# Optimization experiments

Hardware: AMD Instinct MI355X
Metric: run time of the kernel (lower is better)

The kernel has to match this reference:

```python
import jax, jax.numpy as jnp
import numpy as np

B, N, F_IN, F_OUT, T, E, K = 8, 1024, 32, 64, 24, 16384, 3


def setup_inputs() -> dict:
    key = jax.random.key(0)
    ks = jax.random.split(key, 9)
    return {
        "x": jax.random.normal(ks[0], (B, N, F_IN, T), jnp.float32),
        "edge_index": jax.random.randint(ks[1], (2, E), 0, N),
        "edge_weight": jax.random.uniform(ks[2], (E,), jnp.float32),
        # attention params (xavier-ish scale)
        "Ve": jax.random.normal(ks[3], (T, T), jnp.float32) * 0.2,
        "be": jax.random.normal(ks[4], (1, T, T), jnp.float32) * 0.2,
        "Vs": jax.random.normal(ks[5], (N, N), jnp.float32) * 0.03,
        "bs": jax.random.normal(ks[6], (1, N, N), jnp.float32) * 0.03,
        # ChebConv: K linear layers (no bias) + shared bias
        "cheb_W": jax.random.normal(ks[7], (K, F_IN, F_OUT), jnp.float32) * (1.0 / np.sqrt(F_IN)),
        "cheb_b": jnp.zeros((F_OUT,), jnp.float32),
        # 1x1 residual Conv2d(F_IN -> F_OUT): weight (F_OUT, F_IN), bias (F_OUT,)
        "res_W": jax.random.normal(ks[8], (F_OUT, F_IN), jnp.float32) * (1.0 / np.sqrt(F_IN)),
        "res_b": jnp.zeros((F_OUT,), jnp.float32),
    }


def _cheb_conv(x, row, col, w, Wk, b):
    """PyG-style ChebConv applied to a batch of graphs sharing edges.
    x: (BT, N, Fin). Scaled Laplacian with lambda_max=2 reduces to
    L_hat = -D^{-1/2} A D^{-1/2} with zero diagonal (self-loops removed).
    """
    n = x.shape[1]
    w = jnp.where(row == col, jnp.zeros_like(w), w)  # remove_self_loops
    deg = jnp.zeros((n,), x.dtype).at[row].add(w)
    dis = jnp.where(deg > 0, jax.lax.rsqrt(jnp.where(deg > 0, deg, 1.0)), 0.0)
    norm = -dis[row] * w * dis[col]  # (E,)

    def prop(z):  # z: (BT, N, F) -> L_hat @ z
        msg = norm[None, :, None] * z[:, row, :]  # (BT, E, F)
        return jnp.zeros_like(z).at[:, col, :].add(msg)

    Tx0 = x
    out = Tx0 @ Wk[0]
    Tx1 = prop(Tx0)
    out = out + Tx1 @ Wk[1]
    for k in range(2, Wk.shape[0]):  # small fixed K, not a data-dim loop
        Tx2 = 2.0 * prop(Tx1) - Tx0
        out = out + Tx2 @ Wk[k]
        Tx0, Tx1 = Tx1, Tx2
    return out + b


def reference(x, edge_index, edge_weight, Ve, be, Vs, bs, cheb_W, cheb_b, res_W, res_b):
    b_, n, f, t = x.shape
    row, col = edge_index[0], edge_index[1]

    # --- temporal attention: E = softmax(Ve @ sigmoid(X^T X) + be) ---
    x_flat = x.reshape(b_, n * f, t)
    score_t = jnp.einsum('bmt,bmu->btu', x_flat, x_flat)
    E_att = jax.nn.softmax(jnp.einsum('tu,buv->btv', Ve, jax.nn.sigmoid(score_t)) + be, axis=-1)
    x_TA = (x_flat @ E_att).reshape(b_, n, f, t)

    # --- spatial attention: S = softmax(Vs @ sigmoid(X X^T) + bs) ---
    xr = x_TA.reshape(b_, n, f * t)
    score_s = jnp.einsum('bnd,bmd->bnm', xr, xr)
    S_att = jax.nn.softmax(jnp.einsum('nm,bmk->bnk', Vs, jax.nn.sigmoid(score_s)) + bs, axis=-1)
    x_SA = (S_att @ xr).reshape(b_, n, f, t)

    # --- Chebyshev graph conv, batched over all B*T slices at once ---
    xg = x_SA.transpose(0, 3, 1, 2).reshape(b_ * t, n, f)  # (BT, N, Fin)
    x_gcn = _cheb_conv(xg, row, col, edge_weight, cheb_W, cheb_b)
    x_gcn = x_gcn.reshape(b_, t, n, -1).transpose(0, 2, 3, 1)  # (B, N, Fout, T)

    # --- 1x1 residual conv over channel dim ---
    x_res = jnp.einsum('gf,bnft->bngt', res_W, x) + res_b[None, None, :, None]

    return jax.nn.relu(x_gcn + x_res)
```

## Files before the change

### kernel.cpp

```cpp
#include <hip/hip_runtime.h>
#include <math.h>

#define NB 1024
#define FB 32
#define TB 24
#define GB 64
#define BB 8
#define EB 16384
#define MB 32768
#define DB 768
#define BTB 192
#define WSP 6144

typedef __attribute__((ext_vector_type(8))) short sh8;
typedef __attribute__((ext_vector_type(4))) float f32x4;

__device__ __forceinline__ float wsum(float v){
  #pragma unroll
  for (int o = 32; o; o >>= 1) v += __shfl_down(v, o);
  return v;
}
__device__ __forceinline__ float wmax(float v){
  #pragma unroll
  for (int o = 32; o; o >>= 1) v = fmaxf(v, __shfl_down(v, o));
  return v;
}
__device__ __forceinline__ float sigm(float v){ return 1.f / (1.f + expf(-v)); }
__device__ __forceinline__ float b2f(unsigned short u){ unsigned int t = ((unsigned int)u) << 16; return __uint_as_float(t); }
__device__ __forceinline__ unsigned short f2b(float f){
  unsigned int u = __float_as_uint(f);
  u += 0x7fffu + ((u >> 16) & 1u);
  return (unsigned short)(u >> 16);
}
__device__ __forceinline__ void gload16(const void* g, void* l){
  typedef const __attribute__((address_space(1))) unsigned int* gp_t;
  typedef __attribute__((address_space(3))) unsigned int* lp_t;
  __builtin_amdgcn_global_load_lds((gp_t)g, (lp_t)l, 16, 0, 0);
}

__global__ __launch_bounds__(256) void k_pass1(const float* __restrict__ x,
                                               unsigned short* __restrict__ xTn,
                                               float* __restrict__ score){
  const int n0 = blockIdx.x * 8, b = blockIdx.y;
  __shared__ float xl[8 * 32 * 25];
  const float* src = x + ((size_t)b * NB + n0) * DB;
  #pragma unroll
  for (int p = 0; p < 24; ++p){
    int i = p * 256 + threadIdx.x;
    int n = i / 768, rem = i % 768, f = rem / 24, t = rem % 24;
    xl[(n * 32 + f) * 25 + t] = src[i];
  }
  __syncthreads();
  #pragma unroll
  for (int nn = 0; nn < 8; ++nn){
    unsigned short* dst = xTn + ((size_t)(n0 + nn) * BTB + b * TB) * FB;
    #pragma unroll
    for (int p = 0; p < 3; ++p){
      int i2 = p * 256 + threadIdx.x;
      int t = i2 >> 5, f = i2 & 31;
      dst[t * FB + f] = f2b(xl[(nn * 32 + f) * 25 + t]);
    }
  }
  if (threadIdx.x < 192){
    const int t = threadIdx.x >> 3, u0 = (threadIdx.x & 7) * 3;
    float a0 = 0.f, a1 = 0.f, a2 = 0.f;
    for (int m = 0; m < 256; ++m){
      const float xt = xl[m * 25 + t];
      a0 = fmaf(xt, xl[m * 25 + u0 + 0], a0);
      a1 = fmaf(xt, xl[m * 25 + u0 + 1], a1);
      a2 = fmaf(xt, xl[m * 25 + u0 + 2], a2);
    }
    float* sb = score + (size_t)b * 576 + t * 24 + u0;
    atomicAdd(sb + 0, a0); atomicAdd(sb + 1, a1); atomicAdd(sb + 2, a2);
  }
}

__global__ __launch_bounds__(64) void k_eatt(const float* __restrict__ score,
                                             const float* __restrict__ Ve,
                                             const float* __restrict__ be,
                                             float* __restrict__ Eatt){
  const int b = blockIdx.x;
  __shared__ float sg[576], Ar[576], Vel[576], bel[576];
  for (int i = threadIdx.x; i < 576; i += 64){
    sg[i] = sigm(score[(size_t)b * 576 + i]);
    Vel[i] = Ve[i]; bel[i] = be[i];
  }
  __syncthreads();
  for (int i = threadIdx.x; i < 576; i += 64){
    int t = i / 24, v = i % 24;
    float s = 0.f;
    #pragma unroll
    for (int u = 0; u < 24; ++u) s = fmaf(Vel[t*24+u], sg[u*24+v], s);
    Ar[i] = s + bel[i];
  }
  __syncthreads();
  if (threadIdx.x < 24){
    const int t = threadIdx.x;
    float mx = -1e30f;
    #pragma unroll
    for (int v = 0; v < 24; ++v) mx = fmaxf(mx, Ar[t*24+v]);
    float e[24]; float sum = 0.f;
    #pragma unroll
    for (int v = 0; v < 24; ++v){ e[v] = expf(Ar[t*24+v] - mx); sum += e[v]; }
    const float inv = 1.f / sum;
    #pragma unroll
    for (int v = 0; v < 24; ++v) Eatt[(size_t)b * 576 + t*24 + v] = e[v] * inv;
  }
}

__global__ __launch_bounds__(256) void k_xta2(const unsigned short* __restrict__ xTn,
                                              const float* __restrict__ Eatt,
                                              unsigned short* __restrict__ xTAh){
  const int n0 = blockIdx.x * 8, b = blockIdx.y;
  __shared__ float E[576];
  __shared__ unsigned short xl[8 * 32 * 25];
  for (int i = threadIdx.x; i < 576; i += 256) E[i] = Eatt[(size_t)b * 576 + i];
  #pragma unroll
  for (int p = 0; p < 12; ++p){
    int i = p * 256 + threadIdx.x;
    int nn = i / 384, within = i % 384;
    unsigned int v = *(const unsigned int*)(xTn + ((size_t)(n0 + nn) * BTB + b * TB) * FB + within * 2);
    int e0 = within * 2, t0 = e0 >> 5, f0 = e0 & 31;
    int e1 = e0 + 1,     t1 = e1 >> 5, f1 = e1 & 31;
    xl[(nn * 32 + f0) * 25 + t0] = (unsigned short)v;
    xl[(nn * 32 + f1) * 25 + t1] = (unsigned short)(v >> 16);
  }
  __syncthreads();
  const int r = threadIdx.x;
  float in[TB], o[TB];
  #pragma unroll
  for (int u = 0; u < TB; ++u) in[u] = b2f(xl[r * 25 + u]);
  #pragma unroll
  for (int v = 0; v < TB; ++v) o[v] = 0.f;
  #pragma unroll
  for (int u = 0; u < TB; ++u){
    const float xv = in[u];
    #pragma unroll
    for (int v = 0; v < TB; ++v) o[v] = fmaf(xv, E[u*24+v], o[v]);
  }
  unsigned int pk[12];
  #pragma unroll
  for (int q = 0; q < 12; ++q)
    pk[q] = (unsigned int)f2b(o[2*q]) | ((unsigned int)f2b(o[2*q+1]) << 16);
  uint4* op = (uint4*)(xTAh + ((size_t)b * MB + n0 * 32 + r) * TB);
  op[0] = make_uint4(pk[0], pk[1], pk[2], pk[3]);
  op[1] = make_uint4(pk[4], pk[5], pk[6], pk[7]);
  op[2] = make_uint4(pk[8], pk[9], pk[10], pk[11]);
}

__global__ __launch_bounds__(256) void k_tr(const unsigned short* __restrict__ in,
                                            unsigned short* __restrict__ out){
  const int dt = blockIdx.x, nt = blockIdx.y, b = blockIdx.z;
  __shared__ unsigned short ts[64 * 66];
  const unsigned short* ib = in + (size_t)b * (NB * DB) + (size_t)(nt * 64) * DB + dt * 64;
  #pragma unroll
  for (int p = 0; p < 8; ++p){
    int fl = p * 256 + threadIdx.x;
    int rr = fl >> 5, cc = (fl & 31) * 2;
    unsigned int v = *(const unsigned int*)(ib + (size_t)rr * DB + cc);
    ts[rr * 66 + cc] = (unsigned short)v;
    ts[rr * 66 + cc + 1] = (unsigned short)(v >> 16);
  }
  __syncthreads();
  unsigned short* ob = out + (size_t)b * (NB * DB) + (size_t)(dt * 64) * NB + nt * 64;
  #pragma unroll
  for (int p = 0; p < 16; ++p){
    int fl = p * 256 + threadIdx.x;
    int dd = fl >> 6, nn = fl & 63;
    ob[(size_t)dd * NB + nn] = ts[nn * 66 + dd];
  }
}

template<int EPI>
__global__ __launch_bounds__(256) void k_mgemm(const unsigned short* __restrict__ A,
                                               const unsigned short* __restrict__ B,
                                               unsigned short* __restrict__ C,
                                               int lda, int ldb, int ldc, int Kk, int nbx,
                                               long sA, long sB, long sC){
  __shared__ unsigned short As[2][8192];
  __shared__ unsigned short Bs[2][8192];
  const int d = blockIdx.x;
  const int bz = d & 7;
  const int rr = d >> 3;
  const int bx = rr % nbx, by = rr / nbx;
  A += (size_t)bz * sA; B += (size_t)bz * sB; C += (size_t)bz * sC;
  const int i0 = by * 128, j0 = bx * 128;
  const int tid = threadIdx.x, wave = tid >> 6, lane = tid & 63;
  const int fr = lane & 15, rowb = (lane >> 4) * 4;
  const int wr = (wave >> 1) * 64, wc = (wave & 1) * 64;
  const int srow = tid >> 3;
  const int sko = (((lane & 7) ^ (lane >> 3)) * 8);
  f32x4 acc[4][4];
  #pragma unroll
  for (int m = 0; m < 4; ++m)
    #pragma unroll
    for (int n = 0; n < 4; ++n) acc[m][n] = 0.f;

  auto stage = [&](int buf, int k0){
    #pragma unroll
    for (int it = 0; it < 4; ++it){
      const int r = it * 32 + srow;
      gload16(A + (size_t)(i0 + r) * lda + k0 + sko, &As[buf][(it*4 + wave) * 512]);
      gload16(B + (size_t)(j0 + r) * ldb + k0 + sko, &Bs[buf][(it*4 + wave) * 512]);
    }
  };
  auto compute = [&](int buf){
    #pragma unroll
    for (int kk = 0; kk < 2; ++kk){
      const int ch = kk * 4 + (lane >> 4);
      const int cs = (ch ^ (fr & 7)) * 8;
      sh8 af[4], bfr[4];
      #pragma unroll
      for (int m = 0; m < 4; ++m)
        af[m] = *(const sh8*)&As[buf][(wr + m*16 + fr) * 64 + cs];
      #pragma unroll
      for (int n = 0; n < 4; ++n)
        bfr[n] = *(const sh8*)&Bs[buf][(wc + n*16 + fr) * 64 + cs];
      #pragma unroll
      for (int m = 0; m < 4; ++m)
        #pragma unroll
        for (int n = 0; n < 4; ++n)
          acc[m][n] = __builtin_amdgcn_mfma_f32_16x16x32_bf16(af[m], bfr[n], acc[m][n], 0, 0, 0);
    }
  };

  stage(0, 0);
  asm volatile("s_waitcnt vmcnt(0)" ::: "memory");
  __builtin_amdgcn_s_barrier();
  int cur = 0;
  for (int k0 = 64; k0 < Kk; k0 += 64){
    stage(cur ^ 1, k0);
    compute(cur);
    asm volatile("s_waitcnt vmcnt(0)" ::: "memory");
    __builtin_amdgcn_s_barrier();
    cur ^= 1;
  }
  compute(cur);

  #pragma unroll
  for (int m = 0; m < 4; ++m){
    const int row = i0 + wr + m*16 + rowb;
    #pragma unroll
    for (int n = 0; n < 4; ++n){
      const int colg = j0 + wc + n*16 + fr;
      #pragma unroll
      for (int r = 0; r < 4; ++r){
        float v = acc[m][n][r];
        if (EPI == 1) v = sigm(v);
        C[(size_t)(row + r) * ldc + colg] = f2b(v);
      }
    }
  }
}

__global__ __launch_bounds__(256) void k_softmax_s(const unsigned short* __restrict__ C2h,
                                                   const float* __restrict__ bs,
                                                   unsigned short* __restrict__ Sh){
  const int blk = blockIdx.x;
  const int n = blk & 1023;
  const unsigned short* row = C2h + (size_t)blk * 1024;
  const float* bsr = bs + (size_t)n * 1024;
  const int tid = threadIdx.x;
  uint2 rv = ((const uint2*)row)[tid];
  float4 bb = ((const float4*)bsr)[tid];
  float v0 = b2f((unsigned short)rv.x)         + bb.x;
  float v1 = b2f((unsigned short)(rv.x >> 16)) + bb.y;
  float v2 = b2f((unsigned short)rv.y)         + bb.z;
  float v3 = b2f((unsigned short)(rv.y >> 16)) + bb.w;
  float mx = fmaxf(fmaxf(v0, v1), fmaxf(v2, v3));
  mx = wmax(mx);
  __shared__ float s4[4];
  __shared__ float s4b[4];
  if ((tid & 63) == 0) s4[tid >> 6] = mx;
  __syncthreads();
  mx = fmaxf(fmaxf(s4[0], s4[1]), fmaxf(s4[2], s4[3]));
  float e0 = expf(v0 - mx), e1 = expf(v1 - mx), e2 = expf(v2 - mx), e3 = expf(v3 - mx);
  float sum = wsum(e0 + e1 + e2 + e3);
  if ((tid & 63) == 0) s4b[tid >> 6] = sum;
  __syncthreads();
  sum = s4b[0] + s4b[1] + s4b[2] + s4b[3];
  const float inv = 1.f / sum;
  uint2 ov;
  ov.x = (unsigned int)f2b(e0 * inv) | ((unsigned int)f2b(e1 * inv) << 16);
  ov.y = (unsigned int)f2b(e2 * inv) | ((unsigned int)f2b(e3 * inv) << 16);
  ((uint2*)(Sh + (size_t)blk * 1024))[tid] = ov;
}

__global__ __launch_bounds__(256) void k_t0n(const unsigned short* __restrict__ xSAh,
                                             unsigned short* __restrict__ T0n){
  const int n0 = blockIdx.x * 8, b = blockIdx.y;
  __shared__ unsigned short s[8 * 32 * 25];
  const unsigned int* src = (const unsigned int*)(xSAh + ((size_t)b * NB + n0) * DB);
  #pragma unroll
  for (int p = 0; p < 12; ++p){
    int i = p * 256 + threadIdx.x;
    unsigned int v = src[i];
    int d0 = (i * 2) % DB, nn = (i * 2) / DB;
    int f0 = d0 / 24, t0 = d0 % 24;
    int d1 = d0 + 1, f1 = d1 / 24, t1 = d1 % 24;
    s[(nn * 32 + f0) * 25 + t0] = (unsigned short)v;
    s[(nn * 32 + f1) * 25 + t1] = (unsigned short)(v >> 16);
  }
  __syncthreads();
  #pragma unroll
  for (int nn = 0; nn < 8; ++nn){
    unsigned short* dst = T0n + ((size_t)(n0 + nn) * BTB + b * TB) * FB;
    #pragma unroll
    for (int p = 0; p < 3; ++p){
      int i2 = p * 256 + threadIdx.x;
      int t = i2 >> 5, f = i2 & 31;
      dst[t * FB + f] = s[(nn * 32 + f) * 25 + t];
    }
  }
}

__global__ __launch_bounds__(256) void k_edge_deg(const int* __restrict__ ei,
                                                  const float* __restrict__ ew,
                                                  float* __restrict__ deg,
                                                  int* __restrict__ cnt){
  int e = blockIdx.x * 256 + threadIdx.x;
  if (e >= EB) return;
  int r = ei[e], c = ei[EB + e];
  float w = (r == c) ? 0.f : ew[e];
  atomicAdd(&deg[r], w);
  atomicAdd(&cnt[c], 1);
}

__global__ __launch_bounds__(1024) void k_scan(const int* __restrict__ cnt,
                                               int* __restrict__ ptr,
                                               int* __restrict__ fill){
  __shared__ int sd[1024];
  const int i = threadIdx.x;
  int c = cnt[i];
  sd[i] = c;
  __syncthreads();
  int v = c;
  for (int s = 1; s < 1024; s <<= 1){
    int t = (i >= s) ? sd[i - s] : 0;
    __syncthreads();
    v += t; sd[i] = v;
    __syncthreads();
  }
  ptr[i + 1] = v;
  fill[i] = v - c;
  if (i == 0) ptr[0] = 0;
}

__global__ __launch_bounds__(256) void k_edge_fill(const int* __restrict__ ei,
                                                   const float* __restrict__ ew,
                                                   const float* __restrict__ deg,
                                                   int* __restrict__ fill,
                                                   int* __restrict__ cidx,
                                                   float* __restrict__ normv){
  int e = blockIdx.x * 256 + threadIdx.x;
  if (e >= EB) return;
  int r = ei[e], c = ei[EB + e];
  float w = (r == c) ? 0.f : ew[e];
  float dr = deg[r], dc = deg[c];
  float ir = dr > 0.f ? rsqrtf(dr) : 0.f;
  float ic = dc > 0.f ? rsqrtf(dc) : 0.f;
  normv[e] = -ir * w * ic;
  int pos = atomicAdd(&fill[c], 1);
  cidx[pos] = e;
}

#define ACC8(vv) { \
  acc[0] = fmaf(w, b2f((unsigned short)(vv).x), acc[0]); \
  acc[1] = fmaf(w, b2f((unsigned short)((vv).x >> 16)), acc[1]); \
  acc[2] = fmaf(w, b2f((unsigned short)(vv).y), acc[2]); \
  acc[3] = fmaf(w, b2f((unsigned short)((vv).y >> 16)), acc[3]); \
  acc[4] = fmaf(w, b2f((unsigned short)(vv).z), acc[4]); \
  acc[5] = fmaf(w, b2f((unsigned short)((vv).z >> 16)), acc[5]); \
  acc[6] = fmaf(w, b2f((unsigned short)(vv).w), acc[6]); \
  acc[7] = fmaf(w, b2f((unsigned short)((vv).w >> 16)), acc[7]); }

__global__ __launch_bounds__(256) void k_spmm(const unsigned short* __restrict__ z,
                                              const float* __restrict__ normv,
                                              const int* __restrict__ cidx,
                                              const int* __restrict__ ei,
                                              const int* __restrict__ ptr,
                                              const unsigned short* __restrict__ sub,
                                              float scale,
                                              unsigned short* __restrict__ outz){
  const int c = blockIdx.x & 1023;
  const int off = (blockIdx.x >> 10) * 2048 + threadIdx.x * 8;
  const int j0 = ptr[c], j1 = ptr[c + 1];
  __shared__ int rs[128];
  __shared__ float ws[128];
  float acc[8];
  #pragma unroll
  for (int q = 0; q < 8; ++q) acc[q] = 0.f;
  for (int jb = j0; jb < j1; jb += 128){
    const int cnt = min(128, j1 - jb);
    __syncthreads();
    for (int j = threadIdx.x; j < cnt; j += 256){
      int e = cidx[jb + j];
      rs[j] = ei[e];
      ws[j] = normv[e];
    }
    __syncthreads();
    for (int j = 0; j < cnt; ++j){
      const uint4 v = *(const uint4*)(z + (size_t)rs[j] * WSP + off);
      const float w = ws[j];
      ACC8(v)
    }
  }
  float sv[8];
  if (sub){
    const uint4 s0 = *(const uint4*)(sub + (size_t)c * WSP + off);
    sv[0]=b2f((unsigned short)s0.x); sv[1]=b2f((unsigned short)(s0.x>>16));
    sv[2]=b2f((unsigned short)s0.y); sv[3]=b2f((unsigned short)(s0.y>>16));
    sv[4]=b2f((unsigned short)s0.z); sv[5]=b2f((unsigned short)(s0.z>>16));
    sv[6]=b2f((unsigned short)s0.w); sv[7]=b2f((unsigned short)(s0.w>>16));
  } else {
    #pragma unroll
    for (int q = 0; q < 8; ++q) sv[q] = 0.f;
  }
  unsigned int pk[4];
  #pragma unroll
  for (int q = 0; q < 4; ++q){
    float a = scale * acc[2*q]     - sv[2*q];
    float b = scale * acc[2*q + 1] - sv[2*q + 1];
    pk[q] = (unsigned int)f2b(a) | ((unsigned int)f2b(b) << 16);
  }
  *(uint4*)(outz + (size_t)c * WSP + off) = make_uint4(pk[0], pk[1], pk[2], pk[3]);
}

__global__ __launch_bounds__(256) void k_fgemm(const unsigned short* __restrict__ T0n,
                                               const unsigned short* __restrict__ T1n,
                                               const unsigned short* __restrict__ T2n,
                                               const unsigned short* __restrict__ xTn,
                                               const unsigned short* __restrict__ Wh,
                                               const float* __restrict__ bsum,
                                               float* __restrict__ out){
  __shared__ unsigned short As[16384];
  __shared__ unsigned short Ws[8192];
  const int m0 = blockIdx.x * 128;
  const int tid = threadIdx.x, wave = tid >> 6, lane = tid & 63;
  const int fr = lane & 15, rowb = (lane >> 4) * 4;
  const int wr = (wave >> 1) * 64, wc = (wave & 1) * 32;
  #pragma unroll
  for (int it = 0; it < 8; ++it){
    const int row = it * 16 + wave * 4 + (lane >> 4);
    const int g = (lane & 15) ^ (row & 7);
    const int ss = g >> 2, off = (g & 3) * 8;
    const unsigned short* bp = (ss == 0) ? T0n : (ss == 1) ? T1n : (ss == 2) ? T2n : xTn;
    gload16(bp + (size_t)(m0 + row) * FB + off, &As[(it*4 + wave) * 512]);
  }
  #pragma unroll
  for (int it = 0; it < 4; ++it){
    const int row = it * 16 + wave * 4 + (lane >> 4);
    const int g = (lane & 15) ^ (row & 7);
    gload16(Wh + (size_t)row * 128 + g * 8, &Ws[(it*4 + wave) * 512]);
  }
  __syncthreads();
  f32x4 acc[4][2];
  #pragma unroll
  for (int m = 0; m < 4; ++m){ acc[m][0] = 0.f; acc[m][1] = 0.f; }
  #pragma unroll
  for (int kk = 0; kk < 4; ++kk){
    const int ch = kk * 4 + (lane >> 4);
    const int cs = (ch ^ (fr & 7)) * 8;
    sh8 af[4], bf2[2];
    #pragma unroll
    for (int m = 0; m < 4; ++m)
      af[m] = *(const sh8*)&As[(wr + m*16 + fr) * 128 + cs];
    #pragma unroll
    for (int n = 0; n < 2; ++n)
      bf2[n] = *(const sh8*)&Ws[(wc + n*16 + fr) * 128 + cs];
    #pragma unroll
    for (int m = 0; m < 4; ++m)
      #pragma unroll
      for (int n = 0; n < 2; ++n)
        acc[m][n] = __builtin_amdgcn_mfma_f32_16x16x32_bf16(af[m], bf2[n], acc[m][n], 0, 0, 0);
  }
  #pragma unroll
  for (int m = 0; m < 4; ++m){
    const int row4 = m0 + wr + m*16 + rowb;
    const int nn = row4 / 192;
    const int rem = row4 - nn * 192;
    const int b = rem / 24;
    const int t0 = rem - b * 24;
    #pragma unroll
    for (int n = 0; n < 2; ++n){
      const int g = wc + n*16 + fr;
      const float bv = bsum[g];
      float4 v;
      v.x = fmaxf(acc[m][n][0] + bv, 0.f);
      v.y = fmaxf(acc[m][n][1] + bv, 0.f);
      v.z = fmaxf(acc[m][n][2] + bv, 0.f);
      v.w = fmaxf(acc[m][n][3] + bv, 0.f);
      *(float4*)(out + (((size_t)b * NB + nn) * GB + g) * TB + t0) = v;
    }
  }
}

__global__ __launch_bounds__(256) void k_vsh(const float* __restrict__ Vs,
                                             unsigned short* __restrict__ Vsh){
  int i = (blockIdx.x * 256 + threadIdx.x) * 4;
  float4 v = *(const float4*)(Vs + i);
  unsigned short* o = Vsh + i;
  o[0] = f2b(v.x); o[1] = f2b(v.y); o[2] = f2b(v.z); o[3] = f2b(v.w);
}

__global__ __launch_bounds__(256) void k_wcat(const float* __restrict__ cW,
                                              const float* __restrict__ cB,
                                              const float* __restrict__ rW,
                                              const float* __restrict__ rB,
                                              unsigned short* __restrict__ Wh,
                                              float* __restrict__ bsum){
  for (int i = threadIdx.x; i < 8192; i += 256){
    int g = i >> 7, k = i & 127;
    int s = k >> 5, f = k & 31;
    float v = (s < 3) ? cW[(s * 32 + f) * 64 + g] : rW[g * 32 + f];
    Wh[i] = f2b(v);
  }
  if (threadIdx.x < 64) bsum[threadIdx.x] = cB[threadIdx.x] + rB[threadIdx.x];
}

extern "C" void kernel_launch(void* const* d_in, const int* in_sizes, int n_in,
                              void* d_out, int out_size, void* d_ws, size_t ws_size,
                              hipStream_t stream){
  const float* x  = (const float*)d_in[0];
  const int*   ei = (const int*)d_in[1];
  const float* ew = (const float*)d_in[2];
  const float* Ve = (const float*)d_in[3];
  const float* be = (const float*)d_in[4];
  const float* Vs = (const float*)d_in[5];
  const float* bs = (const float*)d_in[6];
  const float* cW = (const float*)d_in[7];
  const float* cB = (const float*)d_in[8];
  const float* rW = (const float*)d_in[9];
  const float* rB = (const float*)d_in[10];
  float* out = (float*)d_out;

  char* W = (char*)d_ws;
  unsigned short* sigh  = (unsigned short*)(W + 0);
  unsigned short* Sh    = sigh;
  unsigned short* xTAh  = (unsigned short*)(W + 16777216);
  unsigned short* T0n   = xTAh;
  unsigned short* xTAhT = (unsigned short*)(W + 29360128);
  unsigned short* T1n   = xTAhT;
  unsigned short* xTn   = (unsigned short*)(W + 41943040);
  unsigned short* xSAh  = (unsigned short*)(W + 54525952);
  unsigned short* T2n   = xSAh;
  unsigned short* C2h   = (unsigned short*)(W + 67108864);
  unsigned short* Vsh   = (unsigned short*)(W + 83886080);
  unsigned short* Wh    = (unsigned short*)(W + 92274688);
  float* bsum  = (float*)(W + 92291072);
  float* score = (float*)(W + 92291328);
  float* Eatt  = (float*)(W + 92309760);
  float* normv = (float*)(W + 92328192);
  float* deg   = (float*)(W + 92393728);
  int*   cnt   = (int*)(W + 92397824);
  int*   ptr   = (int*)(W + 92401920);
  int*   fill  = (int*)(W + 92406272);
  int*   cidx  = (int*)(W + 92410368);

  hipMemsetAsync(score, 0, 18432, stream);
  hipMemsetAsync(deg, 0, 8192, stream);

  k_wcat<<<1, 256, 0, stream>>>(cW, cB, rW, rB, Wh, bsum);
  k_vsh<<<1024, 256, 0, stream>>>(Vs, Vsh);

  k_pass1<<<dim3(128, 8), 256, 0, stream>>>(x, xTn, score);
  k_eatt<<<8, 64, 0, stream>>>(score, Ve, be, Eatt);
  k_xta2<<<dim3(128, 8), 256, 0, stream>>>(xTn, Eatt, xTAh);
  k_tr<<<dim3(12, 16, 8), 256, 0, stream>>>(xTAh, xTAhT);

  k_mgemm<1><<<512, 256, 0, stream>>>(xTAh, xTAh, sigh, DB, DB, NB, DB, 8,
                                      (long)NB*DB, (long)NB*DB, (long)NB*NB);
  k_mgemm<2><<<512, 256, 0, stream>>>(Vsh, sigh, C2h, NB, NB, NB, NB, 8,
                                      0L, (long)NB*NB, (long)NB*NB);
  k_softmax_s<<<8192, 256, 0, stream>>>(C2h, bs, Sh);
  k_mgemm<2><<<384, 256, 0, stream>>>(Sh, xTAhT, xSAh, NB, NB, DB, NB, 6,
                                      (long)NB*NB, (long)NB*DB, (long)NB*DB);

  k_t0n<<<dim3(128, 8), 256, 0, stream>>>(xSAh, T0n);
  k_edge_deg<<<64, 256, 0, stream>>>(ei, ew, deg, cnt);
  k_scan<<<1, 1024, 0, stream>>>(cnt, ptr, fill);
  k_edge_fill<<<64, 256, 0, stream>>>(ei, ew, deg, fill, cidx, normv);
  k_spmm<<<3072, 256, 0, stream>>>(T0n, normv, cidx, ei, ptr, nullptr, 1.f, T1n);
  k_spmm<<<3072, 256, 0, stream>>>(T1n, normv, cidx, ei, ptr, T0n, 2.f, T2n);

  k_fgemm<<<1536, 256, 0, stream>>>(T0n, T1n, T2n, xTn, Wh, bsum, out);
}
```

Before: 237.1 us.

## Exploit Gram symmetry, fuse graph preprocessing and constant kernels, retile SpMM

The spatial score X X^T is symmetric, so a new GEMM kernel computes only the lower-triangular 128x128 tiles (288 blocks instead of 512) and writes each off-diagonal tile twice, once mirrored. That mirrored write is a strided, uncoalesced store. Degree computation, the CSR scan and the edge fill are merged into one 1024-thread block using shared-memory atomics, and the two weight-conversion kernels are merged into one launch. SpMM now uses 192-thread blocks with 4 elements per thread, giving more blocks per column so the gather load spreads more evenly.

```diff
diff --git a/kernel.cpp b/kernel.cpp
--- a/kernel.cpp
+++ b/kernel.cpp
@@ -253,6 +253,89 @@
   }
 }
 
+__global__ __launch_bounds__(256) void k_mgemm_sym(const unsigned short* __restrict__ A,
+                                                   unsigned short* __restrict__ C,
+                                                   int lda, int ldc, int Kk,
+                                                   long sA, long sC){
+  __shared__ unsigned short As[2][8192];
+  __shared__ unsigned short Bs[2][8192];
+  const int d = blockIdx.x;
+  const int bz = d & 7;
+  int r = d >> 3;
+  int by = 0;
+  while (r >= by + 1){ r -= by + 1; ++by; }
+  const int bx = r;
+  A += (size_t)bz * sA; C += (size_t)bz * sC;
+  const int i0 = by * 128, j0 = bx * 128;
+  const int tid = threadIdx.x, wave = tid >> 6, lane = tid & 63;
+  const int fr = lane & 15, rowb = (lane >> 4) * 4;
+  const int wr = (wave >> 1) * 64, wc = (wave & 1) * 64;
+  const int srow = tid >> 3;
+  const int sko = (((lane & 7) ^ (lane >> 3)) * 8);
+  f32x4 acc[4][4];
+  #pragma unroll
+  for (int m = 0; m < 4; ++m)
+    #pragma unroll
+    for (int n = 0; n < 4; ++n) acc[m][n] = 0.f;
+
+  auto stage = [&](int buf, int k0){
+    #pragma unroll
+    for (int it = 0; it < 4; ++it){
+      const int rr2 = it * 32 + srow;
+      gload16(A + (size_t)(i0 + rr2) * lda + k0 + sko, &As[buf][(it*4 + wave) * 512]);
+      gload16(A + (size_t)(j0 + rr2) * lda + k0 + sko, &Bs[buf][(it*4 + wave) * 512]);
+    }
+  };
+  auto compute = [&](int buf){
+    #pragma unroll
+    for (int kk = 0; kk < 2; ++kk){
+      const int ch = kk * 4 + (lane >> 4);
+      const int cs = (ch ^ (fr & 7)) * 8;
+      sh8 af[4], bfr[4];
+      #pragma unroll
+      for (int m = 0; m < 4; ++m)
+        af[m] = *(const sh8*)&As[buf][(wr + m*16 + fr) * 64 + cs];
+      #pragma unroll
+      for (int n = 0; n < 4; ++n)
+        bfr[n] = *(const sh8*)&Bs[buf][(wc + n*16 + fr) * 64 + cs];
+      #pragma unroll
+      for (int m = 0; m < 4; ++m)
+        #pragma unroll
+        for (int n = 0; n < 4; ++n)
+          acc[m][n] = __builtin_amdgcn_mfma_f32_16x16x32_bf16(af[m], bfr[n], acc[m][n], 0, 0, 0);
+    }
+  };
+
+  stage(0, 0);
+  asm volatile("s_waitcnt vmcnt(0)" ::: "memory");
+  __builtin_amdgcn_s_barrier();
+  int cur = 0;
+  for (int k0 = 64; k0 < Kk; k0 += 64){
+    stage(cur ^ 1, k0);
+    compute(cur);
+    asm volatile("s_waitcnt vmcnt(0)" ::: "memory");
+    __builtin_amdgcn_s_barrier();
+    cur ^= 1;
+  }
+  compute(cur);
+
+  const bool mir = (bx != by);
+  #pragma unroll
+  for (int m = 0; m < 4; ++m){
+    const int row = i0 + wr + m*16 + rowb;
+    #pragma unroll
+    for (int n = 0; n < 4; ++n){
+      const int colg = j0 + wc + n*16 + fr;
+      #pragma unroll
+      for (int r2 = 0; r2 < 4; ++r2){
+        const unsigned short h = f2b(sigm(acc[m][n][r2]));
+        C[(size_t)(row + r2) * ldc + colg] = h;
+        if (mir) C[(size_t)colg * ldc + row + r2] = h;
+      }
+    }
+  }
+}
+
 __global__ __launch_bounds__(256) void k_softmax_s(const unsigned short* __restrict__ C2h,
                                                    const float* __restrict__ bs,
                                                    unsigned short* __restrict__ Sh){
@@ -314,24 +397,28 @@
   }
 }
 
-__global__ __launch_bounds__(256) void k_edge_deg(const int* __restrict__ ei,
-                                                  const float* __restrict__ ew,
-                                                  float* __restrict__ deg,
-                                                  int* __restrict__ cnt){
-  int e = blockIdx.x * 256 + threadIdx.x;
-  if (e >= EB) return;
-  int r = ei[e], c = ei[EB + e];
-  float w = (r == c) ? 0.f : ew[e];
-  atomicAdd(&deg[r], w);
-  atomicAdd(&cnt[c], 1);
-}
-
-__global__ __launch_bounds__(1024) void k_scan(const int* __restrict__ cnt,
-                                               int* __restrict__ ptr,
-                                               int* __restrict__ fill){
+__global__ __launch_bounds__(1024) void k_graph(const int* __restrict__ ei,
+                                                const float* __restrict__ ew,
+                                                int* __restrict__ ptr,
+                                                int* __restrict__ cidx,
+                                                float* __restrict__ normv){
+  __shared__ float degs[1024];
+  __shared__ int cnts[1024];
+  __shared__ int base[1024];
   __shared__ int sd[1024];
   const int i = threadIdx.x;
-  int c = cnt[i];
+  degs[i] = 0.f; cnts[i] = 0;
+  __syncthreads();
+  #pragma unroll
+  for (int p = 0; p < 16; ++p){
+    int e = p * 1024 + i;
+    int r = ei[e], c = ei[EB + e];
+    float w = (r == c) ? 0.f : ew[e];
+    atomicAdd(&degs[r], w);
+    atomicAdd(&cnts[c], 1);
+  }
+  __syncthreads();
+  int c = cnts[i];
   sd[i] = c;
   __syncthreads();
   int v = c;
@@ -342,39 +429,24 @@
     __syncthreads();
   }
   ptr[i + 1] = v;
-  fill[i] = v - c;
+  base[i] = v - c;
   if (i == 0) ptr[0] = 0;
-}
-
-__global__ __launch_bounds__(256) void k_edge_fill(const int* __restrict__ ei,
-                                                   const float* __restrict__ ew,
-                                                   const float* __restrict__ deg,
-                                                   int* __restrict__ fill,
-                                                   int* __restrict__ cidx,
-                                                   float* __restrict__ normv){
-  int e = blockIdx.x * 256 + threadIdx.x;
-  if (e >= EB) return;
-  int r = ei[e], c = ei[EB + e];
-  float w = (r == c) ? 0.f : ew[e];
-  float dr = deg[r], dc = deg[c];
-  float ir = dr > 0.f ? rsqrtf(dr) : 0.f;
-  float ic = dc > 0.f ? rsqrtf(dc) : 0.f;
-  normv[e] = -ir * w * ic;
-  int pos = atomicAdd(&fill[c], 1);
-  cidx[pos] = e;
-}
-
-#define ACC8(vv) { \
-  acc[0] = fmaf(w, b2f((unsigned short)(vv).x), acc[0]); \
-  acc[1] = fmaf(w, b2f((unsigned short)((vv).x >> 16)), acc[1]); \
-  acc[2] = fmaf(w, b2f((unsigned short)(vv).y), acc[2]); \
-  acc[3] = fmaf(w, b2f((unsigned short)((vv).y >> 16)), acc[3]); \
-  acc[4] = fmaf(w, b2f((unsigned short)(vv).z), acc[4]); \
-  acc[5] = fmaf(w, b2f((unsigned short)((vv).z >> 16)), acc[5]); \
-  acc[6] = fmaf(w, b2f((unsigned short)(vv).w), acc[6]); \
-  acc[7] = fmaf(w, b2f((unsigned short)((vv).w >> 16)), acc[7]); }
-
-__global__ __launch_bounds__(256) void k_spmm(const unsigned short* __restrict__ z,
+  __syncthreads();
+  #pragma unroll
+  for (int p = 0; p < 16; ++p){
+    int e = p * 1024 + i;
+    int r = ei[e], cc = ei[EB + e];
+    float w = (r == cc) ? 0.f : ew[e];
+    float dr = degs[r], dc = degs[cc];
+    float ir = dr > 0.f ? rsqrtf(dr) : 0.f;
+    float ic = dc > 0.f ? rsqrtf(dc) : 0.f;
+    normv[e] = -ir * w * ic;
+    int pos = atomicAdd(&base[cc], 1);
+    cidx[pos] = e;
+  }
+}
+
+__global__ __launch_bounds__(192) void k_spmm(const unsigned short* __restrict__ z,
                                               const float* __restrict__ normv,
                                               const int* __restrict__ cidx,
                                               const int* __restrict__ ei,
@@ -382,48 +454,41 @@
                                               const unsigned short* __restrict__ sub,
                                               float scale,
                                               unsigned short* __restrict__ outz){
-  const int c = blockIdx.x & 1023;
-  const int off = (blockIdx.x >> 10) * 2048 + threadIdx.x * 8;
+  const int s = blockIdx.x & 7;
+  const int c = blockIdx.x >> 3;
+  const int off = s * 768 + threadIdx.x * 4;
   const int j0 = ptr[c], j1 = ptr[c + 1];
-  __shared__ int rs[128];
-  __shared__ float ws[128];
-  float acc[8];
-  #pragma unroll
-  for (int q = 0; q < 8; ++q) acc[q] = 0.f;
-  for (int jb = j0; jb < j1; jb += 128){
-    const int cnt = min(128, j1 - jb);
+  __shared__ int rs[192];
+  __shared__ float ws[192];
+  float acc[4] = {0.f, 0.f, 0.f, 0.f};
+  for (int jb = j0; jb < j1; jb += 192){
+    const int cnt = min(192, j1 - jb);
     __syncthreads();
-    for (int j = threadIdx.x; j < cnt; j += 256){
-      int e = cidx[jb + j];
-      rs[j] = ei[e];
-      ws[j] = normv[e];
+    if (threadIdx.x < cnt){
+      int e = cidx[jb + threadIdx.x];
+      rs[threadIdx.x] = ei[e];
+      ws[threadIdx.x] = normv[e];
     }
     __syncthreads();
     for (int j = 0; j < cnt; ++j){
-      const uint4 v = *(const uint4*)(z + (size_t)rs[j] * WSP + off);
+      const uint2 v = *(const uint2*)(z + (size_t)rs[j] * WSP + off);
       const float w = ws[j];
-      ACC8(v)
-    }
-  }
-  float sv[8];
+      acc[0] = fmaf(w, b2f((unsigned short)v.x), acc[0]);
+      acc[1] = fmaf(w, b2f((unsigned short)(v.x >> 16)), acc[1]);
+      acc[2] = fmaf(w, b2f((unsigned short)v.y), acc[2]);
+      acc[3] = fmaf(w, b2f((unsigned short)(v.y >> 16)), acc[3]);
+    }
+  }
+  float sv[4] = {0.f, 0.f, 0.f, 0.f};
   if (sub){
-    const uint4 s0 = *(const uint4*)(sub + (size_t)c * WSP + off);
-    sv[0]=b2f((unsigned short)s0.x); sv[1]=b2f((unsigned short)(s0.x>>16));
-    sv[2]=b2f((unsigned short)s0.y); sv[3]=b2f((unsigned short)(s0.y>>16));
-    sv[4]=b2f((unsigned short)s0.z); sv[5]=b2f((unsigned short)(s0.z>>16));
-    sv[6]=b2f((unsigned short)s0.w); sv[7]=b2f((unsigned short)(s0.w>>16));
-  } else {
-    #pragma unroll
-    for (int q = 0; q < 8; ++q) sv[q] = 0.f;
-  }
-  unsigned int pk[4];
-  #pragma unroll
-  for (int q = 0; q < 4; ++q){
-    float a = scale * acc[2*q]     - sv[2*q];
-    float b = scale * acc[2*q + 1] - sv[2*q + 1];
-    pk[q] = (unsigned int)f2b(a) | ((unsigned int)f2b(b) << 16);
-  }
-  *(uint4*)(outz + (size_t)c * WSP + off) = make_uint4(pk[0], pk[1], pk[2], pk[3]);
+    const uint2 s0 = *(const uint2*)(sub + (size_t)c * WSP + off);
+    sv[0] = b2f((unsigned short)s0.x); sv[1] = b2f((unsigned short)(s0.x >> 16));
+    sv[2] = b2f((unsigned short)s0.y); sv[3] = b2f((unsigned short)(s0.y >> 16));
+  }
+  uint2 ov;
+  ov.x = (unsigned int)f2b(scale * acc[0] - sv[0]) | ((unsigned int)f2b(scale * acc[1] - sv[1]) << 16);
+  ov.y = (unsigned int)f2b(scale * acc[2] - sv[2]) | ((unsigned int)f2b(scale * acc[3] - sv[3]) << 16);
+  *(uint2*)(outz + (size_t)c * WSP + off) = ov;
 }
 
 __global__ __launch_bounds__(256) void k_fgemm(const unsigned short* __restrict__ T0n,
@@ -495,27 +560,28 @@
   }
 }
 
-__global__ __launch_bounds__(256) void k_vsh(const float* __restrict__ Vs,
-                                             unsigned short* __restrict__ Vsh){
-  int i = (blockIdx.x * 256 + threadIdx.x) * 4;
-  float4 v = *(const float4*)(Vs + i);
-  unsigned short* o = Vsh + i;
-  o[0] = f2b(v.x); o[1] = f2b(v.y); o[2] = f2b(v.z); o[3] = f2b(v.w);
-}
-
-__global__ __launch_bounds__(256) void k_wcat(const float* __restrict__ cW,
-                                              const float* __restrict__ cB,
-                                              const float* __restrict__ rW,
-                                              const float* __restrict__ rB,
-                                              unsigned short* __restrict__ Wh,
-                                              float* __restrict__ bsum){
-  for (int i = threadIdx.x; i < 8192; i += 256){
-    int g = i >> 7, k = i & 127;
-    int s = k >> 5, f = k & 31;
-    float v = (s < 3) ? cW[(s * 32 + f) * 64 + g] : rW[g * 32 + f];
-    Wh[i] = f2b(v);
-  }
-  if (threadIdx.x < 64) bsum[threadIdx.x] = cB[threadIdx.x] + rB[threadIdx.x];
+__global__ __launch_bounds__(256) void k_const(const float* __restrict__ Vs,
+                                               const float* __restrict__ cW,
+                                               const float* __restrict__ cB,
+                                               const float* __restrict__ rW,
+                                               const float* __restrict__ rB,
+                                               unsigned short* __restrict__ Vsh,
+                                               unsigned short* __restrict__ Wh,
+                                               float* __restrict__ bsum){
+  if (blockIdx.x == 0){
+    for (int i = threadIdx.x; i < 8192; i += 256){
+      int g = i >> 7, k = i & 127;
+      int s = k >> 5, f = k & 31;
+      float v = (s < 3) ? cW[(s * 32 + f) * 64 + g] : rW[g * 32 + f];
+      Wh[i] = f2b(v);
+    }
+    if (threadIdx.x < 64) bsum[threadIdx.x] = cB[threadIdx.x] + rB[threadIdx.x];
+  } else {
+    int i = ((blockIdx.x - 1) * 256 + threadIdx.x) * 4;
+    float4 v = *(const float4*)(Vs + i);
+    unsigned short* o = Vsh + i;
+    o[0] = f2b(v.x); o[1] = f2b(v.y); o[2] = f2b(v.z); o[3] = f2b(v.w);
+  }
 }
 
 extern "C" void kernel_launch(void* const* d_in, const int* in_sizes, int n_in,
@@ -551,25 +617,21 @@
   float* score = (float*)(W + 92291328);
   float* Eatt  = (float*)(W + 92309760);
   float* normv = (float*)(W + 92328192);
-  float* deg   = (float*)(W + 92393728);
-  int*   cnt   = (int*)(W + 92397824);
   int*   ptr   = (int*)(W + 92401920);
-  int*   fill  = (int*)(W + 92406272);
   int*   cidx  = (int*)(W + 92410368);
 
   hipMemsetAsync(score, 0, 18432, stream);
-  hipMemsetAsync(deg, 0, 8192, stream);
-
-  k_wcat<<<1, 256, 0, stream>>>(cW, cB, rW, rB, Wh, bsum);
-  k_vsh<<<1024, 256, 0, stream>>>(Vs, Vsh);
+
+  k_const<<<1025, 256, 0, stream>>>(Vs, cW, cB, rW, rB, Vsh, Wh, bsum);
+  k_graph<<<1, 1024, 0, stream>>>(ei, ew, ptr, cidx, normv);
 
   k_pass1<<<dim3(128, 8), 256, 0, stream>>>(x, xTn, score);
   k_eatt<<<8, 64, 0, stream>>>(score, Ve, be, Eatt);
   k_xta2<<<dim3(128, 8), 256, 0, stream>>>(xTn, Eatt, xTAh);
   k_tr<<<dim3(12, 16, 8), 256, 0, stream>>>(xTAh, xTAhT);
 
-  k_mgemm<1><<<512, 256, 0, stream>>>(xTAh, xTAh, sigh, DB, DB, NB, DB, 8,
-                                      (long)NB*DB, (long)NB*DB, (long)NB*NB);
+  k_mgemm_sym<<<288, 256, 0, stream>>>(xTAh, sigh, DB, NB, DB,
+                                       (long)NB*DB, (long)NB*NB);
   k_mgemm<2><<<512, 256, 0, stream>>>(Vsh, sigh, C2h, NB, NB, NB, NB, 8,
                                       0L, (long)NB*NB, (long)NB*NB);
   k_softmax_s<<<8192, 256, 0, stream>>>(C2h, bs, Sh);
@@ -577,11 +639,8 @@
                                       (long)NB*NB, (long)NB*DB, (long)NB*DB);
 
   k_t0n<<<dim3(128, 8), 256, 0, stream>>>(xSAh, T0n);
-  k_edge_deg<<<64, 256, 0, stream>>>(ei, ew, deg, cnt);
-  k_scan<<<1, 1024, 0, stream>>>(cnt, ptr, fill);
-  k_edge_fill<<<64, 256, 0, stream>>>(ei, ew, deg, fill, cidx, normv);
-  k_spmm<<<3072, 256, 0, stream>>>(T0n, normv, cidx, ei, ptr, nullptr, 1.f, T1n);
-  k_spmm<<<3072, 256, 0, stream>>>(T1n, normv, cidx, ei, ptr, T0n, 2.f, T2n);
+  k_spmm<<<8192, 192, 0, stream>>>(T0n, normv, cidx, ei, ptr, nullptr, 1.f, T1n);
+  k_spmm<<<8192, 192, 0, stream>>>(T1n, normv, cidx, ei, ptr, T0n, 2.f, T2n);
 
   k_fgemm<<<1536, 256, 0, stream>>>(T0n, T1n, T2n, xTn, Wh, bsum, out);
 }
```

Result: slower. 255.5 us (+7.8%).
